# Kernel tuning notes

Hardware: AMD Instinct MI355X
Metric: run time of the kernel (lower is better)

Reference implementation:

```python
import jax, jax.numpy as jnp
import numpy as np

V, H = 32000, 256
B, T_DEC, S_ENC = 32, 64, 64


def setup_inputs() -> dict:
    key = jax.random.key(0)
    ks = jax.random.split(key, 24)
    s = 0.05
    inp = {
        "inputs": jax.random.randint(ks[0], (B, T_DEC), 0, V),
        "annotations": jax.random.normal(ks[1], (B, S_ENC, H), dtype=jnp.float32),
        "hidden_init": jax.random.normal(ks[2], (B, H), dtype=jnp.float32),
        # embedding table
        "emb": jax.random.normal(ks[3], (V, H), dtype=jnp.float32) * s,
        # attention MLP: Linear(2H->H), ReLU, Linear(H->1)
        "W1": jax.random.normal(ks[4], (2 * H, H), dtype=jnp.float32) * s,
        "b1": jnp.zeros((H,), jnp.float32),
        "W2": jax.random.normal(ks[5], (H, 1), dtype=jnp.float32) * s,
        "b2": jnp.zeros((1,), jnp.float32),
        # GRU cell: input_size = 2H
        "Wiz": jax.random.normal(ks[6], (2 * H, H), dtype=jnp.float32) * s,
        "biz": jnp.zeros((H,), jnp.float32),
        "Wir": jax.random.normal(ks[7], (2 * H, H), dtype=jnp.float32) * s,
        "bir": jnp.zeros((H,), jnp.float32),
        "Wih": jax.random.normal(ks[8], (2 * H, H), dtype=jnp.float32) * s,
        "bih": jnp.zeros((H,), jnp.float32),
        "Whz": jax.random.normal(ks[9], (H, H), dtype=jnp.float32) * s,
        "bhz": jnp.zeros((H,), jnp.float32),
        "Whr": jax.random.normal(ks[10], (H, H), dtype=jnp.float32) * s,
        "bhr": jnp.zeros((H,), jnp.float32),
        "Whh": jax.random.normal(ks[11], (H, H), dtype=jnp.float32) * s,
        "bhh": jnp.zeros((H,), jnp.float32),
        # output projection H -> V
        "Wout": jax.random.normal(ks[12], (H, V), dtype=jnp.float32) * s,
        "bout": jnp.zeros((V,), jnp.float32),
    }
    return inp


def reference(inputs, annotations, hidden_init, emb, W1, b1, W2, b2,
              Wiz, biz, Wir, bir, Wih, bih, Whz, bhz, Whr, bhr, Whh, bhh,
              Wout, bout):
    embed = emb[inputs]                      # (B, T, H)
    embed_t = jnp.swapaxes(embed, 0, 1)      # (T, B, H) for scan

    def step(h_prev, x_t):
        # additive attention: queries = h_prev broadcast over enc steps
        q = jnp.broadcast_to(h_prev[:, None, :], annotations.shape)  # (B,S,H)
        pair = jnp.concatenate([q, annotations], axis=2)             # (B,S,2H)
        u = jax.nn.relu(pair @ W1 + b1) @ W2 + b2                    # (B,S,1)
        aw = jax.nn.softmax(u[..., 0], axis=1)                       # (B,S)
        context = jnp.einsum('bs,bsh->bh', aw, annotations)          # (B,H)
        xc = jnp.concatenate([context, x_t], axis=1)                 # (B,2H)
        z = jax.nn.sigmoid(xc @ Wiz + biz + h_prev @ Whz + bhz)
        r = jax.nn.sigmoid(xc @ Wir + bir + h_prev @ Whr + bhr)
        g = jnp.tanh(xc @ Wih + bih + r * (h_prev @ Whh + bhh))
        h_new = (1.0 - z) * g + z * h_prev
        return h_new, (h_new, aw)

    _, (hiddens, attns) = jax.lax.scan(step, hidden_init, embed_t)
    hiddens = jnp.swapaxes(hiddens, 0, 1)      # (B, T, H)
    attentions = jnp.transpose(attns, (1, 2, 0))  # (B, S_enc, T_dec)
    output = hiddens @ Wout + bout             # (B, T, V)
    return output, attentions
```

## Files before the change

### kernel.cpp

```cpp
#include <hip/hip_runtime.h>
#include <hip/hip_bf16.h>

#define Hh 256
#define Ss 64
#define Tt 64
#define Bb 32
#define Vv 32000

typedef __attribute__((ext_vector_type(8))) __bf16 bf16x8;
typedef __attribute__((ext_vector_type(8))) unsigned short u16x8;
typedef __attribute__((ext_vector_type(4))) float f32x4;

__device__ __forceinline__ float bf2f(unsigned short u) {
    union { unsigned int i; float f; } v;
    v.i = ((unsigned int)u) << 16;
    return v.f;
}

__global__ __launch_bounds__(256) void annproj_kernel(
    const float* __restrict__ ann, const float* __restrict__ W1,
    const float* __restrict__ b1, float* __restrict__ annP)
{
    int row = blockIdx.x;
    int tid = threadIdx.x;
    __shared__ float sX[Hh];
    sX[tid] = ann[row * Hh + tid];
    __syncthreads();
    const float* w = W1 + Hh * Hh;
    float acc = b1[tid];
#pragma unroll 4
    for (int i = 0; i < Hh; i++) acc = fmaf(sX[i], w[i * Hh + tid], acc);
    annP[row * Hh + tid] = acc;
}

__global__ __launch_bounds__(256) void embproj_kernel(
    const int* __restrict__ toks, const float* __restrict__ emb,
    const float* __restrict__ Wiz, const float* __restrict__ Wir,
    const float* __restrict__ Wih,
    const float* __restrict__ biz, const float* __restrict__ bir,
    const float* __restrict__ bih,
    const float* __restrict__ bhz, const float* __restrict__ bhr,
    float* __restrict__ eZ, float* __restrict__ eR, float* __restrict__ eH)
{
    int row = blockIdx.x;
    int tid = threadIdx.x;
    __shared__ float sX[Hh];
    sX[tid] = emb[(size_t)toks[row] * Hh + tid];
    __syncthreads();
    const float* wz = Wiz + Hh * Hh;
    const float* wr = Wir + Hh * Hh;
    const float* wh = Wih + Hh * Hh;
    float az = biz[tid] + bhz[tid];
    float ar = bir[tid] + bhr[tid];
    float ah = bih[tid];
#pragma unroll 2
    for (int i = 0; i < Hh; i++) {
        float x = sX[i];
        int o = i * Hh + tid;
        az = fmaf(x, wz[o], az);
        ar = fmaf(x, wr[o], ar);
        ah = fmaf(x, wh[o], ah);
    }
    eZ[row * Hh + tid] = az;
    eR[row * Hh + tid] = ar;
    eH[row * Hh + tid] = ah;
}

__global__ __launch_bounds__(256) void transpose_wout_kernel(
    const float* __restrict__ Wout, __hip_bfloat16* __restrict__ BT)
{
    __shared__ float tile[64][65];
    int n0 = blockIdx.x * 64, k0 = blockIdx.y * 64;
    int tid = threadIdx.x;
    int c = tid & 63, rb = tid >> 6;
#pragma unroll
    for (int it = 0; it < 16; it++) {
        int kk = it * 4 + rb;
        tile[kk][c] = Wout[(size_t)(k0 + kk) * Vv + n0 + c];
    }
    __syncthreads();
#pragma unroll
    for (int it = 0; it < 16; it++) {
        int nn = it * 4 + rb;
        BT[(size_t)(n0 + nn) * Hh + k0 + c] = __float2bfloat16(tile[c][nn]);
    }
}

__global__ __launch_bounds__(256) void pack_weights_kernel(
    const float* __restrict__ W1, const float* __restrict__ Wiz,
    const float* __restrict__ Wir, const float* __restrict__ Wih,
    const float* __restrict__ Whz, const float* __restrict__ Whr,
    const float* __restrict__ Whh, __hip_bfloat16* __restrict__ P)
{
    int c8 = blockIdx.x;
    int m  = blockIdx.y;
    int j  = threadIdx.x;
    const float* src;
    switch (m) {
        case 0: src = W1;  break;
        case 1: src = Wiz; break;
        case 2: src = Wir; break;
        case 3: src = Wih; break;
        case 4: src = Whz; break;
        case 5: src = Whr; break;
        default: src = Whh; break;
    }
    __hip_bfloat16* dst = P + (size_t)m * (Hh * Hh) + ((size_t)c8 * Hh + j) * 8;
#pragma unroll
    for (int d = 0; d < 8; d++)
        dst[d] = __float2bfloat16(src[(c8 * 8 + d) * Hh + j]);
}

__global__ __launch_bounds__(1024) void decoder_kernel(
    const float* __restrict__ ann, const float* __restrict__ h0,
    const __hip_bfloat16* __restrict__ PW,
    const float* __restrict__ W2, const float* __restrict__ b2,
    const float* __restrict__ bhh,
    const float* __restrict__ annP,
    const float* __restrict__ eZ, const float* __restrict__ eR,
    const float* __restrict__ eH,
    __hip_bfloat16* __restrict__ hidBf, float* __restrict__ attOut)
{
    const int b = blockIdx.x, tid = threadIdx.x;
    const int j = tid & 255;
    const int q = tid >> 8;

    __shared__ float sAnnP[Ss][Hh + 1];
    __shared__ float sAnnO[Ss][Hh + 1];
    __shared__ __align__(16) float sH[Hh];
    __shared__ __align__(16) float sHP[Hh];
    __shared__ __align__(16) float sCtx[Hh];
    __shared__ float sW2[Hh];
    __shared__ float sAw[Ss];
    __shared__ float sRedB[16][Ss];
    __shared__ float sRed[16][Hh];

    const u16x8* pW1  = (const u16x8*)(PW);
    const u16x8* pWiz = (const u16x8*)(PW + 1 * 65536);
    const u16x8* pWir = (const u16x8*)(PW + 2 * 65536);
    const u16x8* pWih = (const u16x8*)(PW + 3 * 65536);
    const u16x8* pWhz = (const u16x8*)(PW + 4 * 65536);
    const u16x8* pWhr = (const u16x8*)(PW + 5 * 65536);
    const u16x8* pWhh = (const u16x8*)(PW + 6 * 65536);

    for (int idx = tid; idx < Ss * Hh; idx += 1024) {
        int s = idx >> 8, c = idx & 255;
        sAnnP[s][c] = annP[((size_t)b * Ss + s) * Hh + c];
        sAnnO[s][c] = ann [((size_t)b * Ss + s) * Hh + c];
    }
    if (tid < Hh) { sH[tid] = h0[b * Hh + tid]; sW2[tid] = W2[tid]; }
    const float bhhj = (tid < Hh) ? bhh[tid] : 0.f;
    const float b2s = b2[0];
    const int sphase = tid & 63, cphase = tid >> 6;
    __syncthreads();

    const f32x4* sH4 = (const f32x4*)sH;
    const f32x4* sC4 = (const f32x4*)sCtx;

    for (int t = 0; t < Tt; t++) {
        const int rowt = b * Tt + t;
        float ez = 0.f, er = 0.f, eh = 0.f;
        if (tid < Hh) {
            ez = eZ[(size_t)rowt * Hh + tid];
            er = eR[(size_t)rowt * Hh + tid];
            eh = eH[(size_t)rowt * Hh + tid];
        }

        float pa = 0.f;
#pragma unroll 4
        for (int c = 0; c < 8; c++) {
            int c8 = q * 8 + c;
            u16x8 w = pW1[c8 * Hh + j];
            f32x4 ha = sH4[c8 * 2], hb = sH4[c8 * 2 + 1];
#pragma unroll
            for (int d = 0; d < 4; d++) {
                pa = fmaf(bf2f(w[d]),     ha[d], pa);
                pa = fmaf(bf2f(w[d + 4]), hb[d], pa);
            }
        }
        sRed[q][j] = pa;
        __syncthreads();
        if (tid < Hh)
            sHP[tid] = sRed[0][tid] + sRed[1][tid] + sRed[2][tid] + sRed[3][tid];
        __syncthreads();

        float pb = 0.f;
#pragma unroll
        for (int k = 0; k < 16; k++) {
            int jj = cphase * 16 + k;
            float v = sHP[jj] + sAnnP[sphase][jj];
            pb = fmaf(sW2[jj], fmaxf(v, 0.f), pb);
        }
        sRedB[cphase][sphase] = pb;
        __syncthreads();

        if (tid < 64) {
            float u = b2s;
#pragma unroll
            for (int k = 0; k < 16; k++) u += sRedB[k][tid];
            float m = u;
#pragma unroll
            for (int off = 32; off; off >>= 1) m = fmaxf(m, __shfl_xor(m, off));
            float e = __expf(u - m);
            float ssum = e;
#pragma unroll
            for (int off = 32; off; off >>= 1) ssum += __shfl_xor(ssum, off);
            float aw = e / ssum;
            sAw[tid] = aw;
            attOut[((size_t)b * Ss + tid) * Tt + t] = aw;
        }
        __syncthreads();

        float pd = 0.f;
#pragma unroll
        for (int k = 0; k < 16; k++) {
            int s2 = q * 16 + k;
            pd = fmaf(sAw[s2], sAnnO[s2][j], pd);
        }
        sRed[q][j] = pd;
        __syncthreads();
        if (tid < Hh)
            sCtx[tid] = sRed[0][tid] + sRed[1][tid] + sRed[2][tid] + sRed[3][tid];
        __syncthreads();

        float az = 0.f, ar = 0.f, ah = 0.f, ahh = 0.f;
#pragma unroll 2
        for (int c = 0; c < 8; c++) {
            int c8 = q * 8 + c;
            int widx = c8 * Hh + j;
            u16x8 wz = pWiz[widx], wr = pWir[widx], wh = pWih[widx];
            u16x8 vz = pWhz[widx], vr = pWhr[widx], vh = pWhh[widx];
            f32x4 ca = sC4[c8 * 2], cb = sC4[c8 * 2 + 1];
            f32x4 ga = sH4[c8 * 2], gb = sH4[c8 * 2 + 1];
#pragma unroll
            for (int d = 0; d < 4; d++) {
                float cv = ca[d], hv = ga[d];
                az  = fmaf(bf2f(wz[d]), cv, az);
                az  = fmaf(bf2f(vz[d]), hv, az);
                ar  = fmaf(bf2f(wr[d]), cv, ar);
                ar  = fmaf(bf2f(vr[d]), hv, ar);
                ah  = fmaf(bf2f(wh[d]), cv, ah);
                ahh = fmaf(bf2f(vh[d]), hv, ahh);
            }
#pragma unroll
            for (int d = 0; d < 4; d++) {
                float cv = cb[d], hv = gb[d];
                az  = fmaf(bf2f(wz[d + 4]), cv, az);
                az  = fmaf(bf2f(vz[d + 4]), hv, az);
                ar  = fmaf(bf2f(wr[d + 4]), cv, ar);
                ar  = fmaf(bf2f(vr[d + 4]), hv, ar);
                ah  = fmaf(bf2f(wh[d + 4]), cv, ah);
                ahh = fmaf(bf2f(vh[d + 4]), hv, ahh);
            }
        }
        sRed[q * 4 + 0][j] = az;
        sRed[q * 4 + 1][j] = ar;
        sRed[q * 4 + 2][j] = ah;
        sRed[q * 4 + 3][j] = ahh;
        __syncthreads();

        if (tid < Hh) {
            float accZ  = ez + sRed[0][tid] + sRed[4][tid] + sRed[8][tid]  + sRed[12][tid];
            float accR  = er + sRed[1][tid] + sRed[5][tid] + sRed[9][tid]  + sRed[13][tid];
            float accH  = eh + sRed[2][tid] + sRed[6][tid] + sRed[10][tid] + sRed[14][tid];
            float accHH =      sRed[3][tid] + sRed[7][tid] + sRed[11][tid] + sRed[15][tid];
            float z = 1.f / (1.f + __expf(-accZ));
            float r = 1.f / (1.f + __expf(-accR));
            float g = tanhf(accH + r * (accHH + bhhj));
            float hnew = (1.f - z) * g + z * sH[tid];
            sH[tid] = hnew;
            hidBf[(size_t)rowt * Hh + tid] = __float2bfloat16(hnew);
        }
        __syncthreads();
    }
}

__global__ __launch_bounds__(256) void out_gemm_kernel(
    const __hip_bfloat16* __restrict__ A,
    const __hip_bfloat16* __restrict__ BT,
    const float* __restrict__ bout,
    float* __restrict__ C)
{
    int n0 = blockIdx.x * 128, m0 = blockIdx.y * 128;
    int tid = threadIdx.x;
    int w = tid >> 6, l = tid & 63;
    int wm = (w >> 1) * 64, wn = (w & 1) * 64;
    int quad = l >> 4, l15 = l & 15;

    const __hip_bfloat16* Arow = A + (size_t)(m0 + wm + l15) * Hh + quad * 8;
    const __hip_bfloat16* Brow = BT + (size_t)(n0 + wn + l15) * Hh + quad * 8;

    f32x4 acc[4][4] = {};
#pragma unroll
    for (int kk = 0; kk < 8; kk++) {
        bf16x8 af[4], bfv[4];
#pragma unroll
        for (int mi = 0; mi < 4; mi++)
            af[mi] = *(const bf16x8*)(Arow + mi * 16 * Hh + kk * 32);
#pragma unroll
        for (int ni = 0; ni < 4; ni++)
            bfv[ni] = *(const bf16x8*)(Brow + ni * 16 * Hh + kk * 32);
#pragma unroll
        for (int mi = 0; mi < 4; mi++)
#pragma unroll
            for (int ni = 0; ni < 4; ni++)
                acc[mi][ni] = __builtin_amdgcn_mfma_f32_16x16x32_bf16(
                    af[mi], bfv[ni], acc[mi][ni], 0, 0, 0);
    }
#pragma unroll
    for (int ni = 0; ni < 4; ni++) {
        int col = n0 + wn + ni * 16 + l15;
        float bo = bout[col];
#pragma unroll
        for (int mi = 0; mi < 4; mi++) {
            int rowb = m0 + wm + mi * 16 + quad * 4;
#pragma unroll
            for (int r = 0; r < 4; r++)
                C[(size_t)(rowb + r) * Vv + col] = acc[mi][ni][r] + bo;
        }
    }
}

extern "C" void kernel_launch(void* const* d_in, const int* in_sizes, int n_in,
                              void* d_out, int out_size, void* d_ws, size_t ws_size,
                              hipStream_t stream) {
    const int*   toks = (const int*)d_in[0];
    const float* ann  = (const float*)d_in[1];
    const float* h0   = (const float*)d_in[2];
    const float* emb  = (const float*)d_in[3];
    const float* W1   = (const float*)d_in[4];
    const float* b1   = (const float*)d_in[5];
    const float* W2   = (const float*)d_in[6];
    const float* b2   = (const float*)d_in[7];
    const float* Wiz  = (const float*)d_in[8];
    const float* biz  = (const float*)d_in[9];
    const float* Wir  = (const float*)d_in[10];
    const float* bir  = (const float*)d_in[11];
    const float* Wih  = (const float*)d_in[12];
    const float* bih  = (const float*)d_in[13];
    const float* Whz  = (const float*)d_in[14];
    const float* bhz  = (const float*)d_in[15];
    const float* Whr  = (const float*)d_in[16];
    const float* bhr  = (const float*)d_in[17];
    const float* Whh  = (const float*)d_in[18];
    const float* bhh  = (const float*)d_in[19];
    const float* Wout = (const float*)d_in[20];
    const float* bout = (const float*)d_in[21];

    float* out    = (float*)d_out;
    float* attOut = out + (size_t)Bb * Tt * Vv;

    float* ws   = (float*)d_ws;
    float* annP = ws;
    float* eZ   = ws + 524288;
    float* eR   = ws + 1048576;
    float* eH   = ws + 1572864;
    __hip_bfloat16* hidBf = (__hip_bfloat16*)(ws + 2097152);
    __hip_bfloat16* WoutT = (__hip_bfloat16*)(ws + 2359296);
    __hip_bfloat16* PW    = (__hip_bfloat16*)(ws + 6455296);

    annproj_kernel<<<dim3(Bb * Ss), dim3(256), 0, stream>>>(ann, W1, b1, annP);
    embproj_kernel<<<dim3(Bb * Tt), dim3(256), 0, stream>>>(
        toks, emb, Wiz, Wir, Wih, biz, bir, bih, bhz, bhr, eZ, eR, eH);
    transpose_wout_kernel<<<dim3(Vv / 64, Hh / 64), dim3(256), 0, stream>>>(Wout, WoutT);
    pack_weights_kernel<<<dim3(32, 7), dim3(256), 0, stream>>>(
        W1, Wiz, Wir, Wih, Whz, Whr, Whh, PW);
    decoder_kernel<<<dim3(Bb), dim3(1024), 0, stream>>>(
        ann, h0, PW, W2, b2, bhh, annP, eZ, eR, eH, hidBf, attOut);
    out_gemm_kernel<<<dim3(Vv / 128, (Bb * Tt) / 128), dim3(256), 0, stream>>>(
        hidBf, WoutT, bout, out);
}
```

Measured before the change: 1.196 ms.

## Precompute annotation projections through GRU input weights to skip per-step context matmul

Uses linearity: context@Wi equals aw-weighted sum of (annotations@Wi), so the annotation rows are projected through Wiz/Wir/Wih once up front and stored in bf16 in LDS. Each decoder step then does a 64-term weighted sum instead of a 256x768 matvec, and all four h-dependent matvecs (W1, Whz, Whr, Whh) are fused into one pass with a single reduction. The prep kernels also process several rows per block to reuse weight loads. This trades extra precompute and bf16 rounding of the projected annotations for a shorter serial step chain.

```diff
diff --git a/kernel.cpp b/kernel.cpp
--- a/kernel.cpp
+++ b/kernel.cpp
@@ -17,20 +17,46 @@
     return v.f;
 }
 
-__global__ __launch_bounds__(256) void annproj_kernel(
+__global__ __launch_bounds__(256) void annprep_kernel(
     const float* __restrict__ ann, const float* __restrict__ W1,
-    const float* __restrict__ b1, float* __restrict__ annP)
-{
-    int row = blockIdx.x;
-    int tid = threadIdx.x;
-    __shared__ float sX[Hh];
-    sX[tid] = ann[row * Hh + tid];
+    const float* __restrict__ b1,
+    const float* __restrict__ Wiz, const float* __restrict__ Wir,
+    const float* __restrict__ Wih,
+    __hip_bfloat16* __restrict__ annPb, __hip_bfloat16* __restrict__ annZb,
+    __hip_bfloat16* __restrict__ annRb, __hip_bfloat16* __restrict__ annHb)
+{
+    int row0 = blockIdx.x * 8;
+    int j = threadIdx.x;
+    __shared__ float sX[8][Hh];
+    for (int idx = j; idx < 8 * Hh; idx += 256)
+        sX[idx >> 8][idx & 255] = ann[(size_t)row0 * Hh + idx];
     __syncthreads();
-    const float* w = W1 + Hh * Hh;
-    float acc = b1[tid];
-#pragma unroll 4
-    for (int i = 0; i < Hh; i++) acc = fmaf(sX[i], w[i * Hh + tid], acc);
-    annP[row * Hh + tid] = acc;
+    const float* w1b = W1 + Hh * Hh;
+    float aP[8], aZ[8], aR[8], aH[8];
+    float b1j = b1[j];
+#pragma unroll
+    for (int r = 0; r < 8; r++) { aP[r] = b1j; aZ[r] = 0.f; aR[r] = 0.f; aH[r] = 0.f; }
+#pragma unroll 2
+    for (int i = 0; i < Hh; i++) {
+        int o = i * Hh + j;
+        float w1v = w1b[o], wzv = Wiz[o], wrv = Wir[o], whv = Wih[o];
+#pragma unroll
+        for (int r = 0; r < 8; r++) {
+            float x = sX[r][i];
+            aP[r] = fmaf(x, w1v, aP[r]);
+            aZ[r] = fmaf(x, wzv, aZ[r]);
+            aR[r] = fmaf(x, wrv, aR[r]);
+            aH[r] = fmaf(x, whv, aH[r]);
+        }
+    }
+#pragma unroll
+    for (int r = 0; r < 8; r++) {
+        size_t o = (size_t)(row0 + r) * Hh + j;
+        annPb[o] = __float2bfloat16(aP[r]);
+        annZb[o] = __float2bfloat16(aZ[r]);
+        annRb[o] = __float2bfloat16(aR[r]);
+        annHb[o] = __float2bfloat16(aH[r]);
+    }
 }
 
 __global__ __launch_bounds__(256) void embproj_kernel(
@@ -42,28 +68,40 @@
     const float* __restrict__ bhz, const float* __restrict__ bhr,
     float* __restrict__ eZ, float* __restrict__ eR, float* __restrict__ eH)
 {
-    int row = blockIdx.x;
+    int row0 = blockIdx.x * 4;
     int tid = threadIdx.x;
-    __shared__ float sX[Hh];
-    sX[tid] = emb[(size_t)toks[row] * Hh + tid];
+    __shared__ float sX[4][Hh];
+#pragma unroll
+    for (int r = 0; r < 4; r++)
+        sX[r][tid] = emb[(size_t)toks[row0 + r] * Hh + tid];
     __syncthreads();
     const float* wz = Wiz + Hh * Hh;
     const float* wr = Wir + Hh * Hh;
     const float* wh = Wih + Hh * Hh;
-    float az = biz[tid] + bhz[tid];
-    float ar = bir[tid] + bhr[tid];
-    float ah = bih[tid];
+    float bz = biz[tid] + bhz[tid];
+    float br = bir[tid] + bhr[tid];
+    float bh = bih[tid];
+    float az[4], ar4[4], ah[4];
+#pragma unroll
+    for (int r = 0; r < 4; r++) { az[r] = bz; ar4[r] = br; ah[r] = bh; }
 #pragma unroll 2
     for (int i = 0; i < Hh; i++) {
-        float x = sX[i];
         int o = i * Hh + tid;
-        az = fmaf(x, wz[o], az);
-        ar = fmaf(x, wr[o], ar);
-        ah = fmaf(x, wh[o], ah);
-    }
-    eZ[row * Hh + tid] = az;
-    eR[row * Hh + tid] = ar;
-    eH[row * Hh + tid] = ah;
+        float vz = wz[o], vr = wr[o], vh = wh[o];
+#pragma unroll
+        for (int r = 0; r < 4; r++) {
+            float x = sX[r][i];
+            az[r]  = fmaf(x, vz, az[r]);
+            ar4[r] = fmaf(x, vr, ar4[r]);
+            ah[r]  = fmaf(x, vh, ah[r]);
+        }
+    }
+#pragma unroll
+    for (int r = 0; r < 4; r++) {
+        eZ[(size_t)(row0 + r) * Hh + tid] = az[r];
+        eR[(size_t)(row0 + r) * Hh + tid] = ar4[r];
+        eH[(size_t)(row0 + r) * Hh + tid] = ah[r];
+    }
 }
 
 __global__ __launch_bounds__(256) void transpose_wout_kernel(
@@ -86,11 +124,10 @@
     }
 }
 
-__global__ __launch_bounds__(256) void pack_weights_kernel(
-    const float* __restrict__ W1, const float* __restrict__ Wiz,
-    const float* __restrict__ Wir, const float* __restrict__ Wih,
-    const float* __restrict__ Whz, const float* __restrict__ Whr,
-    const float* __restrict__ Whh, __hip_bfloat16* __restrict__ P)
+__global__ __launch_bounds__(256) void pack4_kernel(
+    const float* __restrict__ W1, const float* __restrict__ Whz,
+    const float* __restrict__ Whr, const float* __restrict__ Whh,
+    __hip_bfloat16* __restrict__ PW)
 {
     int c8 = blockIdx.x;
     int m  = blockIdx.y;
@@ -98,25 +135,25 @@
     const float* src;
     switch (m) {
         case 0: src = W1;  break;
-        case 1: src = Wiz; break;
-        case 2: src = Wir; break;
-        case 3: src = Wih; break;
-        case 4: src = Whz; break;
-        case 5: src = Whr; break;
+        case 1: src = Whz; break;
+        case 2: src = Whr; break;
         default: src = Whh; break;
     }
-    __hip_bfloat16* dst = P + (size_t)m * (Hh * Hh) + ((size_t)c8 * Hh + j) * 8;
+    __hip_bfloat16* dst = PW + (((size_t)m * 32 + c8) * Hh + j) * 8;
 #pragma unroll
     for (int d = 0; d < 8; d++)
         dst[d] = __float2bfloat16(src[(c8 * 8 + d) * Hh + j]);
 }
 
 __global__ __launch_bounds__(1024) void decoder_kernel(
-    const float* __restrict__ ann, const float* __restrict__ h0,
+    const float* __restrict__ h0,
     const __hip_bfloat16* __restrict__ PW,
     const float* __restrict__ W2, const float* __restrict__ b2,
     const float* __restrict__ bhh,
-    const float* __restrict__ annP,
+    const __hip_bfloat16* __restrict__ annPb,
+    const __hip_bfloat16* __restrict__ annZb,
+    const __hip_bfloat16* __restrict__ annRb,
+    const __hip_bfloat16* __restrict__ annHb,
     const float* __restrict__ eZ, const float* __restrict__ eR,
     const float* __restrict__ eH,
     __hip_bfloat16* __restrict__ hidBf, float* __restrict__ attOut)
@@ -125,79 +162,102 @@
     const int j = tid & 255;
     const int q = tid >> 8;
 
-    __shared__ float sAnnP[Ss][Hh + 1];
-    __shared__ float sAnnO[Ss][Hh + 1];
-    __shared__ __align__(16) float sH[Hh];
-    __shared__ __align__(16) float sHP[Hh];
-    __shared__ __align__(16) float sCtx[Hh];
-    __shared__ float sW2[Hh];
-    __shared__ float sAw[Ss];
+    __shared__ unsigned short lZ[Ss * Hh];
+    __shared__ unsigned short lR[Ss * Hh];
+    __shared__ unsigned short lHt[Ss * Hh];
+    __shared__ unsigned short lP[Ss][Hh + 2];
+    __shared__ float sRed[16][Hh];
+    __shared__ float sLoc[4][Hh];
     __shared__ float sRedB[16][Ss];
-    __shared__ float sRed[16][Hh];
-
-    const u16x8* pW1  = (const u16x8*)(PW);
-    const u16x8* pWiz = (const u16x8*)(PW + 1 * 65536);
-    const u16x8* pWir = (const u16x8*)(PW + 2 * 65536);
-    const u16x8* pWih = (const u16x8*)(PW + 3 * 65536);
-    const u16x8* pWhz = (const u16x8*)(PW + 4 * 65536);
-    const u16x8* pWhr = (const u16x8*)(PW + 5 * 65536);
-    const u16x8* pWhh = (const u16x8*)(PW + 6 * 65536);
-
-    for (int idx = tid; idx < Ss * Hh; idx += 1024) {
-        int s = idx >> 8, c = idx & 255;
-        sAnnP[s][c] = annP[((size_t)b * Ss + s) * Hh + c];
-        sAnnO[s][c] = ann [((size_t)b * Ss + s) * Hh + c];
-    }
-    if (tid < Hh) { sH[tid] = h0[b * Hh + tid]; sW2[tid] = W2[tid]; }
-    const float bhhj = (tid < Hh) ? bhh[tid] : 0.f;
+    __shared__ float awLoc[Ss];
+    __shared__ __align__(16) float hLoc[Hh];
+    __shared__ float w2Loc[Hh];
+
+    {
+        u16x8* dZ = (u16x8*)lZ;  const u16x8* sZ = (const u16x8*)(annZb + (size_t)b * Ss * Hh);
+        u16x8* dR = (u16x8*)lR;  const u16x8* sR = (const u16x8*)(annRb + (size_t)b * Ss * Hh);
+        u16x8* dH = (u16x8*)lHt; const u16x8* sHsrc = (const u16x8*)(annHb + (size_t)b * Ss * Hh);
+        for (int idx = tid; idx < Ss * Hh / 8; idx += 1024) {
+            dZ[idx] = sZ[idx]; dR[idx] = sR[idx]; dH[idx] = sHsrc[idx];
+        }
+        const unsigned short* sP = (const unsigned short*)(annPb + (size_t)b * Ss * Hh);
+        for (int idx = tid; idx < Ss * Hh; idx += 1024)
+            lP[idx >> 8][idx & 255] = sP[idx];
+        if (tid < Hh) { hLoc[tid] = h0[b * Hh + tid]; w2Loc[tid] = W2[tid]; }
+    }
+    const float rbhh = (tid < Hh) ? bhh[j] : 0.f;
     const float b2s = b2[0];
-    const int sphase = tid & 63, cphase = tid >> 6;
     __syncthreads();
 
-    const f32x4* sH4 = (const f32x4*)sH;
-    const f32x4* sC4 = (const f32x4*)sCtx;
+    const f32x4* h4 = (const f32x4*)hLoc;
+    const u16x8* pw = (const u16x8*)PW;
 
     for (int t = 0; t < Tt; t++) {
         const int rowt = b * Tt + t;
+
         float ez = 0.f, er = 0.f, eh = 0.f;
         if (tid < Hh) {
-            ez = eZ[(size_t)rowt * Hh + tid];
-            er = eR[(size_t)rowt * Hh + tid];
-            eh = eH[(size_t)rowt * Hh + tid];
-        }
-
-        float pa = 0.f;
-#pragma unroll 4
-        for (int c = 0; c < 8; c++) {
-            int c8 = q * 8 + c;
-            u16x8 w = pW1[c8 * Hh + j];
-            f32x4 ha = sH4[c8 * 2], hb = sH4[c8 * 2 + 1];
-#pragma unroll
-            for (int d = 0; d < 4; d++) {
-                pa = fmaf(bf2f(w[d]),     ha[d], pa);
-                pa = fmaf(bf2f(w[d + 4]), hb[d], pa);
+            ez = eZ[(size_t)rowt * Hh + j];
+            er = eR[(size_t)rowt * Hh + j];
+            eh = eH[(size_t)rowt * Hh + j];
+        }
+
+        {
+            float hp = 0.f, hz = 0.f, hr = 0.f, hh = 0.f;
+#pragma unroll 2
+            for (int c = 0; c < 8; c++) {
+                int c8 = q * 8 + c;
+                int o = c8 * Hh + j;
+                u16x8 w0 = pw[o], w1 = pw[8192 + o], w2v = pw[16384 + o], w3 = pw[24576 + o];
+                f32x4 ha = h4[c8 * 2], hb = h4[c8 * 2 + 1];
+#pragma unroll
+                for (int d = 0; d < 4; d++) {
+                    float x = ha[d];
+                    hp = fmaf(bf2f(w0[d]), x, hp);
+                    hz = fmaf(bf2f(w1[d]), x, hz);
+                    hr = fmaf(bf2f(w2v[d]), x, hr);
+                    hh = fmaf(bf2f(w3[d]), x, hh);
+                }
+#pragma unroll
+                for (int d = 0; d < 4; d++) {
+                    float x = hb[d];
+                    hp = fmaf(bf2f(w0[d + 4]), x, hp);
+                    hz = fmaf(bf2f(w1[d + 4]), x, hz);
+                    hr = fmaf(bf2f(w2v[d + 4]), x, hr);
+                    hh = fmaf(bf2f(w3[d + 4]), x, hh);
+                }
             }
-        }
-        sRed[q][j] = pa;
-        __syncthreads();
-        if (tid < Hh)
-            sHP[tid] = sRed[0][tid] + sRed[1][tid] + sRed[2][tid] + sRed[3][tid];
-        __syncthreads();
-
-        float pb = 0.f;
-#pragma unroll
-        for (int k = 0; k < 16; k++) {
-            int jj = cphase * 16 + k;
-            float v = sHP[jj] + sAnnP[sphase][jj];
-            pb = fmaf(sW2[jj], fmaxf(v, 0.f), pb);
-        }
-        sRedB[cphase][sphase] = pb;
+            sRed[q * 4 + 0][j] = hp;
+            sRed[q * 4 + 1][j] = hz;
+            sRed[q * 4 + 2][j] = hr;
+            sRed[q * 4 + 3][j] = hh;
+        }
+        __syncthreads();
+
+        {
+            int st = tid >> 8, jj = tid & 255;
+            sLoc[st][jj] = sRed[st][jj] + sRed[4 + st][jj] +
+                           sRed[8 + st][jj] + sRed[12 + st][jj];
+        }
+        __syncthreads();
+
+        {
+            int s = tid & 63, g = tid >> 6;
+            float pb = 0.f;
+#pragma unroll
+            for (int kk = 0; kk < 16; kk++) {
+                int jj = g * 16 + kk;
+                float v = sLoc[0][jj] + bf2f(lP[s][jj]);
+                pb = fmaf(w2Loc[jj], fmaxf(v, 0.f), pb);
+            }
+            sRedB[g][s] = pb;
+        }
         __syncthreads();
 
         if (tid < 64) {
             float u = b2s;
 #pragma unroll
-            for (int k = 0; k < 16; k++) u += sRedB[k][tid];
+            for (int g = 0; g < 16; g++) u += sRedB[g][tid];
             float m = u;
 #pragma unroll
             for (int off = 32; off; off >>= 1) m = fmaxf(m, __shfl_xor(m, off));
@@ -206,70 +266,38 @@
 #pragma unroll
             for (int off = 32; off; off >>= 1) ssum += __shfl_xor(ssum, off);
             float aw = e / ssum;
-            sAw[tid] = aw;
+            awLoc[tid] = aw;
             attOut[((size_t)b * Ss + tid) * Tt + t] = aw;
         }
         __syncthreads();
 
-        float pd = 0.f;
-#pragma unroll
-        for (int k = 0; k < 16; k++) {
-            int s2 = q * 16 + k;
-            pd = fmaf(sAw[s2], sAnnO[s2][j], pd);
-        }
-        sRed[q][j] = pd;
-        __syncthreads();
-        if (tid < Hh)
-            sCtx[tid] = sRed[0][tid] + sRed[1][tid] + sRed[2][tid] + sRed[3][tid];
-        __syncthreads();
-
-        float az = 0.f, ar = 0.f, ah = 0.f, ahh = 0.f;
-#pragma unroll 2
-        for (int c = 0; c < 8; c++) {
-            int c8 = q * 8 + c;
-            int widx = c8 * Hh + j;
-            u16x8 wz = pWiz[widx], wr = pWir[widx], wh = pWih[widx];
-            u16x8 vz = pWhz[widx], vr = pWhr[widx], vh = pWhh[widx];
-            f32x4 ca = sC4[c8 * 2], cb = sC4[c8 * 2 + 1];
-            f32x4 ga = sH4[c8 * 2], gb = sH4[c8 * 2 + 1];
-#pragma unroll
-            for (int d = 0; d < 4; d++) {
-                float cv = ca[d], hv = ga[d];
-                az  = fmaf(bf2f(wz[d]), cv, az);
-                az  = fmaf(bf2f(vz[d]), hv, az);
-                ar  = fmaf(bf2f(wr[d]), cv, ar);
-                ar  = fmaf(bf2f(vr[d]), hv, ar);
-                ah  = fmaf(bf2f(wh[d]), cv, ah);
-                ahh = fmaf(bf2f(vh[d]), hv, ahh);
+        {
+            float az = 0.f, ar = 0.f, ah = 0.f;
+#pragma unroll
+            for (int k2 = 0; k2 < 16; k2++) {
+                int s = q * 16 + k2;
+                float a = awLoc[s];
+                int o = s * Hh + j;
+                az = fmaf(a, bf2f(lZ[o]), az);
+                ar = fmaf(a, bf2f(lR[o]), ar);
+                ah = fmaf(a, bf2f(lHt[o]), ah);
             }
-#pragma unroll
-            for (int d = 0; d < 4; d++) {
-                float cv = cb[d], hv = gb[d];
-                az  = fmaf(bf2f(wz[d + 4]), cv, az);
-                az  = fmaf(bf2f(vz[d + 4]), hv, az);
-                ar  = fmaf(bf2f(wr[d + 4]), cv, ar);
-                ar  = fmaf(bf2f(vr[d + 4]), hv, ar);
-                ah  = fmaf(bf2f(wh[d + 4]), cv, ah);
-                ahh = fmaf(bf2f(vh[d + 4]), hv, ahh);
-            }
-        }
-        sRed[q * 4 + 0][j] = az;
-        sRed[q * 4 + 1][j] = ar;
-        sRed[q * 4 + 2][j] = ah;
-        sRed[q * 4 + 3][j] = ahh;
+            sRed[q][j]     = az;
+            sRed[4 + q][j] = ar;
+            sRed[8 + q][j] = ah;
+        }
         __syncthreads();
 
         if (tid < Hh) {
-            float accZ  = ez + sRed[0][tid] + sRed[4][tid] + sRed[8][tid]  + sRed[12][tid];
-            float accR  = er + sRed[1][tid] + sRed[5][tid] + sRed[9][tid]  + sRed[13][tid];
-            float accH  = eh + sRed[2][tid] + sRed[6][tid] + sRed[10][tid] + sRed[14][tid];
-            float accHH =      sRed[3][tid] + sRed[7][tid] + sRed[11][tid] + sRed[15][tid];
-            float z = 1.f / (1.f + __expf(-accZ));
-            float r = 1.f / (1.f + __expf(-accR));
-            float g = tanhf(accH + r * (accHH + bhhj));
-            float hnew = (1.f - z) * g + z * sH[tid];
-            sH[tid] = hnew;
-            hidBf[(size_t)rowt * Hh + tid] = __float2bfloat16(hnew);
+            float sumZ = sRed[0][j] + sRed[1][j] + sRed[2][j] + sRed[3][j];
+            float sumR = sRed[4][j] + sRed[5][j] + sRed[6][j] + sRed[7][j];
+            float sumH = sRed[8][j] + sRed[9][j] + sRed[10][j] + sRed[11][j];
+            float z = 1.f / (1.f + __expf(-(ez + sLoc[1][j] + sumZ)));
+            float r = 1.f / (1.f + __expf(-(er + sLoc[2][j] + sumR)));
+            float g = tanhf(eh + sumH + r * (sLoc[3][j] + rbhh));
+            float hnew = (1.f - z) * g + z * hLoc[j];
+            hLoc[j] = hnew;
+            hidBf[(size_t)rowt * Hh + j] = __float2bfloat16(hnew);
         }
         __syncthreads();
     }
@@ -350,23 +378,27 @@
     float* out    = (float*)d_out;
     float* attOut = out + (size_t)Bb * Tt * Vv;
 
-    float* ws   = (float*)d_ws;
-    float* annP = ws;
-    float* eZ   = ws + 524288;
-    float* eR   = ws + 1048576;
-    float* eH   = ws + 1572864;
-    __hip_bfloat16* hidBf = (__hip_bfloat16*)(ws + 2097152);
-    __hip_bfloat16* WoutT = (__hip_bfloat16*)(ws + 2359296);
-    __hip_bfloat16* PW    = (__hip_bfloat16*)(ws + 6455296);
-
-    annproj_kernel<<<dim3(Bb * Ss), dim3(256), 0, stream>>>(ann, W1, b1, annP);
-    embproj_kernel<<<dim3(Bb * Tt), dim3(256), 0, stream>>>(
+    float* ws = (float*)d_ws;
+    float* eZ = ws;
+    float* eR = ws + 524288;
+    float* eH = ws + 1048576;
+    __hip_bfloat16* hidBf = (__hip_bfloat16*)(ws + 1572864);
+    __hip_bfloat16* WoutT = (__hip_bfloat16*)(ws + 1835008);
+    __hip_bfloat16* annPb = (__hip_bfloat16*)(ws + 5931008);
+    __hip_bfloat16* annZb = (__hip_bfloat16*)(ws + 6193152);
+    __hip_bfloat16* annRb = (__hip_bfloat16*)(ws + 6455296);
+    __hip_bfloat16* annHb = (__hip_bfloat16*)(ws + 6717440);
+    __hip_bfloat16* PW    = (__hip_bfloat16*)(ws + 6979584);
+
+    annprep_kernel<<<dim3(Bb * Ss / 8), dim3(256), 0, stream>>>(
+        ann, W1, b1, Wiz, Wir, Wih, annPb, annZb, annRb, annHb);
+    embproj_kernel<<<dim3(Bb * Tt / 4), dim3(256), 0, stream>>>(
         toks, emb, Wiz, Wir, Wih, biz, bir, bih, bhz, bhr, eZ, eR, eH);
     transpose_wout_kernel<<<dim3(Vv / 64, Hh / 64), dim3(256), 0, stream>>>(Wout, WoutT);
-    pack_weights_kernel<<<dim3(32, 7), dim3(256), 0, stream>>>(
-        W1, Wiz, Wir, Wih, Whz, Whr, Whh, PW);
+    pack4_kernel<<<dim3(32, 4), dim3(256), 0, stream>>>(W1, Whz, Whr, Whh, PW);
     decoder_kernel<<<dim3(Bb), dim3(1024), 0, stream>>>(
-        ann, h0, PW, W2, b2, bhh, annP, eZ, eR, eH, hidBf, attOut);
+        h0, PW, W2, b2, bhh, annPb, annZb, annRb, annHb,
+        eZ, eR, eH, hidBf, attOut);
     out_gemm_kernel<<<dim3(Vv / 128, (Bb * Tt) / 128), dim3(256), 0, stream>>>(
         hidBf, WoutT, bout, out);
 }
```

Result: faster. 1.134 ms (-5.2%).
